# Performance work log

Measured on AMD Instinct MI355X. Metric: run time of the kernel, lower is better.

Reference implementation:

```python
import jax, jax.numpy as jnp
import numpy as np

B, Q, D = 4, 1024, 1024
N, DH = 16, 64  # n_head, d_head
SCALE = 1.0 / DH ** 0.5
LN_EPS = 1e-5


def setup_inputs() -> dict:
    key = jax.random.key(0)
    ks = jax.random.split(key, 10)
    return {
        "w": jax.random.normal(ks[0], (B, Q, D), jnp.float32),
        "r_emb": jax.random.normal(ks[1], (Q, N, DH), jnp.float32),
        "r_w_bias": jax.random.normal(ks[2], (N, DH), jnp.float32),
        "r_bias": jax.random.normal(ks[3], (Q, N), jnp.float32),
        # projection weights stored [in, out]; torch Linear init std = 1/sqrt(d_head)
        "Wq": jax.random.normal(ks[4], (D, N * DH), jnp.float32) * SCALE,
        "Wk": jax.random.normal(ks[5], (D, N * DH), jnp.float32) * SCALE,
        "Wv": jax.random.normal(ks[6], (D, N * DH), jnp.float32) * SCALE,
        "Wo": jax.random.normal(ks[7], (N * DH, D), jnp.float32) * SCALE,
        "ln_gamma": jnp.ones((D,), jnp.float32),
        "ln_beta": jnp.zeros((D,), jnp.float32),
    }


def _rel_shift(x):
    # x: [b, i, j, n]; pad a zero column at the end of j then drop j=0
    # equivalent to shifting left by one along j with a trailing zero.
    return jnp.concatenate([x[:, :, 1:, :], jnp.zeros_like(x[:, :, :1, :])], axis=2)


def reference(w, r_emb, r_w_bias, r_bias, Wq, Wk, Wv, Wo, ln_gamma, ln_beta):
    b, qlen, d = w.shape
    klen = qlen  # mems=None
    n, dh = r_w_bias.shape

    q_h = (w @ Wq).reshape(b, qlen, n, dh)
    k_h = (w @ Wk).reshape(b, klen, n, dh)
    v_h = (w @ Wv).reshape(b, klen, n, dh)

    rw_q = q_h + r_w_bias[None, None]                      # [b,q,n,dh]
    AC = jnp.einsum('bind,bjnd->bijn', rw_q, k_h)          # [b,q,k,n]
    B_ = jnp.einsum('bind,jnd->bijn', q_h, r_emb)          # [b,q,k,n]
    BD = _rel_shift(B_ + r_bias[None, None])               # [b,q,k,n]

    attn_score = (AC + BD) * SCALE
    attn_prob = jax.nn.softmax(attn_score, axis=2)
    attn_vec = jnp.einsum('bijn,bjnd->bind', attn_prob, v_h)
    attn_out = attn_vec.reshape(b, qlen, n * dh) @ Wo

    out = w + attn_out  # residual (post-lnorm path)
    mu = jnp.mean(out, axis=-1, keepdims=True)
    var = jnp.var(out, axis=-1, keepdims=True)
    return (out - mu) / jnp.sqrt(var + LN_EPS) * ln_gamma + ln_beta
```

## Files before the change

kernel.cpp:

```cpp
#include <hip/hip_runtime.h>
#include <hip/hip_bf16.h>

using f16 = _Float16;
typedef _Float16 f16x8 __attribute__((ext_vector_type(8)));
typedef _Float16 f16x4 __attribute__((ext_vector_type(4)));
typedef float f32x4 __attribute__((ext_vector_type(4)));

#define AS1 __attribute__((address_space(1)))
#define AS3 __attribute__((address_space(3)))

constexpr int Bc = 4, Qc = 1024, Dc = 1024, Nh = 16, DHc = 64;
constexpr int BQ = Bc * Qc;
constexpr int NHEAD = Bc * Nh;
constexpr float ATT_SCALE = 0.125f;

__global__ void k_f2h(const float* __restrict__ src, f16* __restrict__ dst) {
    long i8 = ((long)blockIdx.x * blockDim.x + threadIdx.x) * 8;
    float4 a = *(const float4*)&src[i8];
    float4 b = *(const float4*)&src[i8 + 4];
    f16x8 o = { (f16)a.x, (f16)a.y, (f16)a.z, (f16)a.w,
                (f16)b.x, (f16)b.y, (f16)b.z, (f16)b.w };
    *(f16x8*)&dst[i8] = o;
}

struct Ptr4 { const float* p[4]; };
__global__ void k_transpose4(Ptr4 srcs, f16* __restrict__ dst) {
    __shared__ f16 tile[32][33];
    const float* src = srcs.p[blockIdx.z];
    f16* d = dst + (long)blockIdx.z * Dc * Dc;
    int c0 = blockIdx.x * 32, r0 = blockIdx.y * 32;
#pragma unroll
    for (int dy = 0; dy < 32; dy += 8) {
        int r = r0 + threadIdx.y + dy, c = c0 + threadIdx.x;
        tile[threadIdx.y + dy][threadIdx.x] = (f16)src[(long)r * Dc + c];
    }
    __syncthreads();
#pragma unroll
    for (int dy = 0; dy < 32; dy += 8) {
        int c = c0 + threadIdx.y + dy, r = r0 + threadIdx.x;
        d[(long)c * Dc + r] = tile[threadIdx.x][threadIdx.y + dy];
    }
}

__global__ void k_fill_remb(const float* __restrict__ remb, f16* __restrict__ Ke) {
    long gid = (long)blockIdx.x * blockDim.x + threadIdx.x;
    int d8 = (int)(gid & 7) * 8;
    int j = (int)((gid >> 3) & 1023);
    int h = (int)(gid >> 13);
    int n = h & 15;
    f16x8 kv;
    if (j < 1023) {
        const float* rp = &remb[((long)(j + 1) * 16 + n) * 64 + d8];
        float4 r0 = *(const float4*)rp, r1 = *(const float4*)(rp + 4);
        kv[0] = (f16)r0.x; kv[1] = (f16)r0.y; kv[2] = (f16)r0.z; kv[3] = (f16)r0.w;
        kv[4] = (f16)r1.x; kv[5] = (f16)r1.y; kv[6] = (f16)r1.z; kv[7] = (f16)r1.w;
    } else {
        kv = f16x8{};
    }
    *(f16x8*)&Ke[(((long)h << 10) + j) * 64 + d8] = kv;
}

template <int BM, int BN, int BK, int WROWS, int WCOLS, int EPI>
__global__ __launch_bounds__(256) void k_gemm_nt(
    const f16* __restrict__ A, const f16* __restrict__ Bt, void* __restrict__ Cv,
    f16* __restrict__ qtp, f16* __restrict__ ktp, f16* __restrict__ vtp,
    int lda, int ldb, int ldc, int K)
{
    constexpr int TM = BM / (WROWS * 16);
    constexpr int TN = BN / (WCOLS * 16);
    __shared__ __align__(16) f16 sA[BM * BK];
    __shared__ __align__(16) f16 sB[BN * BK];

    const int tid = threadIdx.x;
    const int lane = tid & 63, wave = tid >> 6;
    const int wm = wave / WCOLS, wn = wave % WCOLS;
    const int m0 = blockIdx.y * BM, n0 = blockIdx.x * BN;

    f32x4 acc[TM][TN] = {};

    const int lrow = lane & 15;
    const int kq = (lane >> 4) * 8;
    const int srow = lane >> 2;
    const int scol = (lane & 3) * 8;

    for (int k0 = 0; k0 < K; k0 += BK) {
        __syncthreads();
        constexpr int CHA = BM * BK / 512;
#pragma unroll
        for (int ch = 0; ch < CHA / 4; ++ch) {
            int cc = ch * 4 + wave;
            __builtin_amdgcn_global_load_lds(
                (const AS1 void*)(const void*)&A[(long)(m0 + cc * 16 + srow) * lda + k0 + scol],
                (AS3 void*)(void*)&sA[cc * 512], 16, 0, 0);
        }
        constexpr int CHB = BN * BK / 512;
#pragma unroll
        for (int ch = 0; ch < CHB / 4; ++ch) {
            int cc = ch * 4 + wave;
            __builtin_amdgcn_global_load_lds(
                (const AS1 void*)(const void*)&Bt[(long)(n0 + cc * 16 + srow) * ldb + k0 + scol],
                (AS3 void*)(void*)&sB[cc * 512], 16, 0, 0);
        }
        __syncthreads();

        f16x8 af[TM], bfr[TN];
#pragma unroll
        for (int mi = 0; mi < TM; ++mi)
            af[mi] = *(const f16x8*)&sA[(wm * TM * 16 + mi * 16 + lrow) * BK + kq];
#pragma unroll
        for (int ni = 0; ni < TN; ++ni)
            bfr[ni] = *(const f16x8*)&sB[(wn * TN * 16 + ni * 16 + lrow) * BK + kq];
#pragma unroll
        for (int mi = 0; mi < TM; ++mi)
#pragma unroll
            for (int ni = 0; ni < TN; ++ni)
                acc[mi][ni] = __builtin_amdgcn_mfma_f32_16x16x32_f16(af[mi], bfr[ni], acc[mi][ni], 0, 0, 0);
    }

    const int crow = (lane >> 4) * 4;
    const int ccol = lane & 15;
#pragma unroll
    for (int mi = 0; mi < TM; ++mi)
#pragma unroll
        for (int ni = 0; ni < TN; ++ni)
#pragma unroll
            for (int r = 0; r < 4; ++r) {
                int gm = m0 + wm * TM * 16 + mi * 16 + crow + r;
                int gn = n0 + wn * TN * 16 + ni * 16 + ccol;
                float val = acc[mi][ni][r];
                if constexpr (EPI == 0) {
                    ((f16*)Cv)[(long)gm * ldc + gn] = (f16)val;
                } else {
                    int seg = n0 >> 10;
                    int col = gn & 1023;
                    if (seg == 0) {
                        qtp[(long)gm * 1024 + col] = (f16)val;
                    } else if (seg == 1) {
                        ktp[(long)gm * 1024 + col] = (f16)val;
                    } else {
                        int b = gm >> 10, i = gm & 1023;
                        vtp[(((long)(b << 10) + col) << 10) + i] = (f16)val;
                    }
                }
            }
}

__global__ __launch_bounds__(256, 2) void k_flash(
    const f16* __restrict__ qh, const f16* __restrict__ kh,
    const f16* __restrict__ Ke, const f16* __restrict__ vT,
    const float* __restrict__ rwb, const float* __restrict__ r_bias,
    f16* __restrict__ avp)
{
    constexpr int LDL = 136;
    __shared__ __align__(16) f16 sK[128 * LDL];
    __shared__ __align__(16) f16 sV[64 * LDL];
    __shared__ float sRB[128];

    const int tid = threadIdx.x, lane = tid & 63, wave = tid >> 6;
    const int bid = blockIdx.x;
    const int h = (((bid >> 3) & 7) << 3) | (bid & 7);
    const int i0 = (bid >> 6) * 128;
    const int b = h >> 4, n = h & 15;

    const f16* Vh = vT + (long)h * DHc * Qc;

    const int lrow = lane & 15;
    const int quad = lane >> 4;

    f16x8 rw0, rw1;
#pragma unroll
    for (int e = 0; e < 8; ++e) {
        rw0[e] = (f16)rwb[n * 64 + quad * 8 + e];
        rw1[e] = (f16)rwb[n * 64 + 32 + quad * 8 + e];
    }

    f16x8 aq[2][4];
#pragma unroll
    for (int t = 0; t < 2; ++t) {
        long rix = (long)(b * Qc + i0 + wave * 32 + t * 16 + lrow) * 1024 + n * 64;
        f16x8 q0 = *(const f16x8*)&qh[rix + quad * 8];
        f16x8 q1 = *(const f16x8*)&qh[rix + 32 + quad * 8];
        aq[t][0] = q0 + rw0;
        aq[t][1] = q1 + rw1;
        aq[t][2] = q0;
        aq[t][3] = q1;
    }

    float m_i[2] = {-1e30f, -1e30f}, l_i[2] = {0.0f, 0.0f};
    f32x4 o_acc[2][4] = {};

    for (int j0 = 0; j0 < Qc; j0 += 128) {
        __syncthreads();
        for (int idx = tid; idx < 1024; idx += 256) {
            int r = idx >> 3, c = (idx & 7) * 8;
            *(uint4*)&sK[r * LDL + c] =
                *(const uint4*)&kh[(long)(b * Qc + j0 + r) * 1024 + n * 64 + c];
            *(uint4*)&sK[r * LDL + 64 + c] =
                *(const uint4*)&Ke[((long)h * Qc + j0 + r) * 64 + c];
        }
        for (int idx = tid; idx < 64 * 16; idx += 256) {
            int r = idx >> 4, c = (idx & 15) * 8;
            *(uint4*)&sV[r * LDL + c] = *(const uint4*)&Vh[(long)r * Qc + j0 + c];
        }
        if (tid < 128) {
            int j = j0 + tid;
            sRB[tid] = (j < Qc - 1) ? r_bias[(j + 1) * Nh + n] : 0.0f;
        }
        __syncthreads();

        f32x4 s_acc[2][8] = {};
#pragma unroll
        for (int kc = 0; kc < 4; ++kc)
#pragma unroll
            for (int ni = 0; ni < 8; ++ni) {
                f16x8 bk = *(const f16x8*)&sK[(ni * 16 + lrow) * LDL + kc * 32 + quad * 8];
                s_acc[0][ni] = __builtin_amdgcn_mfma_f32_16x16x32_f16(bk, aq[0][kc], s_acc[0][ni], 0, 0, 0);
                s_acc[1][ni] = __builtin_amdgcn_mfma_f32_16x16x32_f16(bk, aq[1][kc], s_acc[1][ni], 0, 0, 0);
            }

        f16x4 pf[2][8];
        float alpha_t[2];
#pragma unroll
        for (int t = 0; t < 2; ++t) {
            float mx = -1e30f;
#pragma unroll
            for (int ni = 0; ni < 8; ++ni) {
                f32x4 rb4 = *(const f32x4*)&sRB[ni * 16 + quad * 4];
#pragma unroll
                for (int r = 0; r < 4; ++r) {
                    float v = (s_acc[t][ni][r] + rb4[r]) * ATT_SCALE;
                    s_acc[t][ni][r] = v;
                    mx = fmaxf(mx, v);
                }
            }
            mx = fmaxf(mx, __shfl_xor(mx, 16));
            mx = fmaxf(mx, __shfl_xor(mx, 32));
            float mn = fmaxf(m_i[t], mx);
            float alpha = __expf(m_i[t] - mn);
            float sm = 0.0f;
#pragma unroll
            for (int ni = 0; ni < 8; ++ni) {
                float e0 = __expf(s_acc[t][ni][0] - mn);
                float e1 = __expf(s_acc[t][ni][1] - mn);
                float e2 = __expf(s_acc[t][ni][2] - mn);
                float e3 = __expf(s_acc[t][ni][3] - mn);
                sm += (e0 + e1) + (e2 + e3);
                f16x4 pvv; pvv[0] = (f16)e0; pvv[1] = (f16)e1; pvv[2] = (f16)e2; pvv[3] = (f16)e3;
                pf[t][ni] = pvv;
            }
            sm += __shfl_xor(sm, 16);
            sm += __shfl_xor(sm, 32);
            l_i[t] = l_i[t] * alpha + sm;
            m_i[t] = mn;
            alpha_t[t] = alpha;
        }

#pragma unroll
        for (int t = 0; t < 2; ++t)
#pragma unroll
            for (int r = 0; r < 4; ++r) {
                float al = __shfl(alpha_t[t], quad * 4 + r);
#pragma unroll
                for (int dt = 0; dt < 4; ++dt) o_acc[t][dt][r] *= al;
            }

#pragma unroll
        for (int nj = 0; nj < 8; ++nj)
#pragma unroll
            for (int dt = 0; dt < 4; ++dt) {
                f16x4 bv = *(const f16x4*)&sV[(dt * 16 + lrow) * LDL + nj * 16 + quad * 4];
                o_acc[0][dt] = __builtin_amdgcn_mfma_f32_16x16x16f16(pf[0][nj], bv, o_acc[0][dt], 0, 0, 0);
                o_acc[1][dt] = __builtin_amdgcn_mfma_f32_16x16x16f16(pf[1][nj], bv, o_acc[1][dt], 0, 0, 0);
            }
    }

#pragma unroll
    for (int t = 0; t < 2; ++t) {
        float linv = 1.0f / l_i[t];
#pragma unroll
        for (int r = 0; r < 4; ++r) {
            float li = __shfl(linv, quad * 4 + r);
            int i = i0 + wave * 32 + t * 16 + quad * 4 + r;
#pragma unroll
            for (int dt = 0; dt < 4; ++dt) {
                int d = dt * 16 + lrow;
                avp[((long)(b * Qc + i) << 10) + n * 64 + d] = (f16)(o_acc[t][dt][r] * li);
            }
        }
    }
}

__global__ __launch_bounds__(256) void k_res_ln(const float* __restrict__ w, const f16* __restrict__ ao,
                                                const float* __restrict__ gamma, const float* __restrict__ beta,
                                                float* __restrict__ out) {
    const long base = (long)blockIdx.x * 1024;
    const int tid = threadIdx.x;
    float4 wv = *(const float4*)&w[base + tid * 4];
    f16x4 av = *(const f16x4*)&ao[base + tid * 4];
    float x[4] = { wv.x + (float)av[0], wv.y + (float)av[1],
                   wv.z + (float)av[2], wv.w + (float)av[3] };
    float s = x[0] + x[1] + x[2] + x[3];
    float s2 = x[0] * x[0] + x[1] * x[1] + x[2] * x[2] + x[3] * x[3];
#pragma unroll
    for (int off = 32; off; off >>= 1) { s += __shfl_down(s, off); s2 += __shfl_down(s2, off); }
    __shared__ float rs[4], rs2[4];
    if ((tid & 63) == 0) { rs[tid >> 6] = s; rs2[tid >> 6] = s2; }
    __syncthreads();
    s = rs[0] + rs[1] + rs[2] + rs[3];
    s2 = rs2[0] + rs2[1] + rs2[2] + rs2[3];
    float mu = s * (1.0f / 1024.0f);
    float var = s2 * (1.0f / 1024.0f) - mu * mu;
    float inv = rsqrtf(var + 1e-5f);
    float4 gv = *(const float4*)&gamma[tid * 4];
    float4 bv = *(const float4*)&beta[tid * 4];
    float4 o;
    o.x = (x[0] - mu) * inv * gv.x + bv.x;
    o.y = (x[1] - mu) * inv * gv.y + bv.y;
    o.z = (x[2] - mu) * inv * gv.z + bv.z;
    o.w = (x[3] - mu) * inv * gv.w + bv.w;
    *(float4*)&out[base + tid * 4] = o;
}

extern "C" void kernel_launch(void* const* d_in, const int* in_sizes, int n_in,
                              void* d_out, int out_size, void* d_ws, size_t ws_size,
                              hipStream_t stream) {
    const float* w_in   = (const float*)d_in[0];
    const float* r_emb  = (const float*)d_in[1];
    const float* r_wb   = (const float*)d_in[2];
    const float* r_bias = (const float*)d_in[3];
    const float* Wq     = (const float*)d_in[4];
    const float* Wk     = (const float*)d_in[5];
    const float* Wv     = (const float*)d_in[6];
    const float* Wo     = (const float*)d_in[7];
    const float* ln_g   = (const float*)d_in[8];
    const float* ln_b   = (const float*)d_in[9];
    float* out = (float*)d_out;

    char* p = (char*)d_ws;
    auto alloc = [&](size_t bytes) { char* r = p; p += (bytes + 255) & ~(size_t)255; return r; };
    f16* wh = (f16*)alloc((size_t)BQ * Dc * 2);
    f16* WT = (f16*)alloc((size_t)4 * Dc * Dc * 2);
    f16* qh = (f16*)alloc((size_t)BQ * Dc * 2);
    f16* kh = (f16*)alloc((size_t)BQ * Dc * 2);
    f16* Ke = (f16*)alloc((size_t)NHEAD * Qc * DHc * 2);
    f16* vT = (f16*)alloc((size_t)BQ * Dc * 2);
    f16* WoT = WT + (size_t)3 * Dc * Dc;
    f16* avp = wh;
    f16* ao  = Ke;

    k_f2h<<<(BQ * Dc) / (256 * 8), 256, 0, stream>>>(w_in, wh);

    Ptr4 srcs{{Wq, Wk, Wv, Wo}};
    k_transpose4<<<dim3(32, 32, 4), dim3(32, 8), 0, stream>>>(srcs, WT);

    k_fill_remb<<<(NHEAD * Qc * 8) / 256, 256, 0, stream>>>(r_emb, Ke);

    k_gemm_nt<128, 128, 32, 2, 2, 5><<<dim3(3 * Dc / 128, BQ / 128), 256, 0, stream>>>(
        wh, WT, nullptr, qh, kh, vT, Dc, Dc, 0, Dc);

    k_flash<<<512, 256, 0, stream>>>(qh, kh, Ke, vT, r_wb, r_bias, avp);

    k_gemm_nt<64, 128, 32, 2, 2, 0><<<dim3(Dc / 128, BQ / 64), 256, 0, stream>>>(
        avp, WoT, ao, nullptr, nullptr, nullptr, Dc, Dc, Dc, Dc);

    k_res_ln<<<BQ, 256, 0, stream>>>(w_in, ao, ln_g, ln_b, out);
}
```

Baseline: 225.7 us.

## Prefetch next K/V tile into registers during attention compute; fold scale into Q

The attention loop now issues global loads for the next K, Ke, V and r_bias tile into registers before computing on the current tile, then writes them to LDS after the PV MFMAs. This lets global memory latency overlap with compute instead of stalling at the top of each iteration. The softmax scale is also folded into Q, r_w_bias and r_bias, which removes a per-score multiply. The cost is extra registers (12 uint4 per thread), which may reduce occupancy. Scaling Q in fp16 may also change rounding slightly.

Measured after the change: 256.4 us. +13.6%, slower.

```diff
diff --git a/kernel.cpp b/kernel.cpp
--- a/kernel.cpp
+++ b/kernel.cpp
@@ -170,43 +170,76 @@
     f16x8 rw0, rw1;
 #pragma unroll
     for (int e = 0; e < 8; ++e) {
-        rw0[e] = (f16)rwb[n * 64 + quad * 8 + e];
-        rw1[e] = (f16)rwb[n * 64 + 32 + quad * 8 + e];
-    }
-
+        rw0[e] = (f16)(rwb[n * 64 + quad * 8 + e] * ATT_SCALE);
+        rw1[e] = (f16)(rwb[n * 64 + 32 + quad * 8 + e] * ATT_SCALE);
+    }
+
+    const f16 qsc = (f16)0.125f;
     f16x8 aq[2][4];
 #pragma unroll
     for (int t = 0; t < 2; ++t) {
         long rix = (long)(b * Qc + i0 + wave * 32 + t * 16 + lrow) * 1024 + n * 64;
-        f16x8 q0 = *(const f16x8*)&qh[rix + quad * 8];
-        f16x8 q1 = *(const f16x8*)&qh[rix + 32 + quad * 8];
+        f16x8 q0 = *(const f16x8*)&qh[rix + quad * 8] * qsc;
+        f16x8 q1 = *(const f16x8*)&qh[rix + 32 + quad * 8] * qsc;
         aq[t][0] = q0 + rw0;
         aq[t][1] = q1 + rw1;
         aq[t][2] = q0;
         aq[t][3] = q1;
     }
 
+    uint4 rk0[4], rk1[4], rv[4];
+    float rbv;
+
+    auto issue_loads = [&](int j0) {
+#pragma unroll
+        for (int it = 0; it < 4; ++it) {
+            int idx = tid + it * 256;
+            int r = idx >> 3, c = (idx & 7) * 8;
+            rk0[it] = *(const uint4*)&kh[(long)(b * Qc + j0 + r) * 1024 + n * 64 + c];
+            rk1[it] = *(const uint4*)&Ke[((long)h * Qc + j0 + r) * 64 + c];
+        }
+#pragma unroll
+        for (int it = 0; it < 4; ++it) {
+            int idx = tid + it * 256;
+            int r = idx >> 4, c = (idx & 15) * 8;
+            rv[it] = *(const uint4*)&Vh[(long)r * Qc + j0 + c];
+        }
+        rbv = 0.0f;
+        if (tid < 128) {
+            int j = j0 + tid;
+            rbv = (j < Qc - 1) ? r_bias[(j + 1) * Nh + n] * ATT_SCALE : 0.0f;
+        }
+    };
+    auto write_lds = [&]() {
+#pragma unroll
+        for (int it = 0; it < 4; ++it) {
+            int idx = tid + it * 256;
+            int r = idx >> 3, c = (idx & 7) * 8;
+            *(uint4*)&sK[r * LDL + c] = rk0[it];
+            *(uint4*)&sK[r * LDL + 64 + c] = rk1[it];
+        }
+#pragma unroll
+        for (int it = 0; it < 4; ++it) {
+            int idx = tid + it * 256;
+            int r = idx >> 4, c = (idx & 15) * 8;
+            *(uint4*)&sV[r * LDL + c] = rv[it];
+        }
+        if (tid < 128) sRB[tid] = rbv;
+    };
+
     float m_i[2] = {-1e30f, -1e30f}, l_i[2] = {0.0f, 0.0f};
     f32x4 o_acc[2][4] = {};
 
+    issue_loads(0);
+    write_lds();
+    __syncthreads();
+
     for (int j0 = 0; j0 < Qc; j0 += 128) {
-        __syncthreads();
-        for (int idx = tid; idx < 1024; idx += 256) {
-            int r = idx >> 3, c = (idx & 7) * 8;
-            *(uint4*)&sK[r * LDL + c] =
-                *(const uint4*)&kh[(long)(b * Qc + j0 + r) * 1024 + n * 64 + c];
-            *(uint4*)&sK[r * LDL + 64 + c] =
-                *(const uint4*)&Ke[((long)h * Qc + j0 + r) * 64 + c];
-        }
-        for (int idx = tid; idx < 64 * 16; idx += 256) {
-            int r = idx >> 4, c = (idx & 15) * 8;
-            *(uint4*)&sV[r * LDL + c] = *(const uint4*)&Vh[(long)r * Qc + j0 + c];
-        }
-        if (tid < 128) {
-            int j = j0 + tid;
-            sRB[tid] = (j < Qc - 1) ? r_bias[(j + 1) * Nh + n] : 0.0f;
-        }
-        __syncthreads();
+        const bool has_next = (j0 + 128) < Qc;
+        if (has_next) {
+            issue_loads(j0 + 128);
+            __builtin_amdgcn_sched_barrier(0);
+        }
 
         f32x4 s_acc[2][8] = {};
 #pragma unroll
@@ -228,7 +261,7 @@
                 f32x4 rb4 = *(const f32x4*)&sRB[ni * 16 + quad * 4];
 #pragma unroll
                 for (int r = 0; r < 4; ++r) {
-                    float v = (s_acc[t][ni][r] + rb4[r]) * ATT_SCALE;
+                    float v = s_acc[t][ni][r] + rb4[r];
                     s_acc[t][ni][r] = v;
                     mx = fmaxf(mx, v);
                 }
@@ -272,6 +305,12 @@
                 o_acc[0][dt] = __builtin_amdgcn_mfma_f32_16x16x16f16(pf[0][nj], bv, o_acc[0][dt], 0, 0, 0);
                 o_acc[1][dt] = __builtin_amdgcn_mfma_f32_16x16x16f16(pf[1][nj], bv, o_acc[1][dt], 0, 0, 0);
             }
+
+        if (has_next) {
+            __syncthreads();
+            write_lds();
+            __syncthreads();
+        }
     }
 
 #pragma unroll
```

## Split flash attention across 8 waves with 16 query rows each, prefold scale

Applied to the files above, without the earlier changes.

The flash-attention block grows from 4 waves to 8 waves. Each wave now handles 16 query rows instead of 32, which halves the per-wave accumulator and score registers and raises occupancy. The softmax scale is folded into Q, into r_w_bias and into r_bias ahead of time, which removes one multiply per score element. In exchange, each K/V tile is reused by fewer MFMA calls per wave, and the scale is applied in fp16 before the dot product, which changes rounding slightly.

Measured after the change: 218.6 us. 3.1% less time.

```diff
diff --git a/kernel.cpp b/kernel.cpp
--- a/kernel.cpp
+++ b/kernel.cpp
@@ -145,7 +145,7 @@
             }
 }
 
-__global__ __launch_bounds__(256, 2) void k_flash(
+__global__ __launch_bounds__(512, 4) void k_flash(
     const f16* __restrict__ qh, const f16* __restrict__ kh,
     const f16* __restrict__ Ke, const f16* __restrict__ vT,
     const float* __restrict__ rwb, const float* __restrict__ r_bias,
@@ -170,121 +170,111 @@
     f16x8 rw0, rw1;
 #pragma unroll
     for (int e = 0; e < 8; ++e) {
-        rw0[e] = (f16)rwb[n * 64 + quad * 8 + e];
-        rw1[e] = (f16)rwb[n * 64 + 32 + quad * 8 + e];
-    }
-
-    f16x8 aq[2][4];
-#pragma unroll
-    for (int t = 0; t < 2; ++t) {
-        long rix = (long)(b * Qc + i0 + wave * 32 + t * 16 + lrow) * 1024 + n * 64;
-        f16x8 q0 = *(const f16x8*)&qh[rix + quad * 8];
-        f16x8 q1 = *(const f16x8*)&qh[rix + 32 + quad * 8];
-        aq[t][0] = q0 + rw0;
-        aq[t][1] = q1 + rw1;
-        aq[t][2] = q0;
-        aq[t][3] = q1;
-    }
-
-    float m_i[2] = {-1e30f, -1e30f}, l_i[2] = {0.0f, 0.0f};
-    f32x4 o_acc[2][4] = {};
+        rw0[e] = (f16)(rwb[n * 64 + quad * 8 + e] * ATT_SCALE);
+        rw1[e] = (f16)(rwb[n * 64 + 32 + quad * 8 + e] * ATT_SCALE);
+    }
+
+    const f16 qsc = (f16)0.125f;
+    f16x8 aq[4];
+    {
+        long rix = (long)(b * Qc + i0 + wave * 16 + lrow) * 1024 + n * 64;
+        f16x8 q0 = *(const f16x8*)&qh[rix + quad * 8] * qsc;
+        f16x8 q1 = *(const f16x8*)&qh[rix + 32 + quad * 8] * qsc;
+        aq[0] = q0 + rw0;
+        aq[1] = q1 + rw1;
+        aq[2] = q0;
+        aq[3] = q1;
+    }
+
+    float m_i = -1e30f, l_i = 0.0f;
+    f32x4 o_acc[4] = {};
 
     for (int j0 = 0; j0 < Qc; j0 += 128) {
         __syncthreads();
-        for (int idx = tid; idx < 1024; idx += 256) {
+        for (int idx = tid; idx < 1024; idx += 512) {
             int r = idx >> 3, c = (idx & 7) * 8;
             *(uint4*)&sK[r * LDL + c] =
                 *(const uint4*)&kh[(long)(b * Qc + j0 + r) * 1024 + n * 64 + c];
             *(uint4*)&sK[r * LDL + 64 + c] =
                 *(const uint4*)&Ke[((long)h * Qc + j0 + r) * 64 + c];
         }
-        for (int idx = tid; idx < 64 * 16; idx += 256) {
+        for (int idx = tid; idx < 64 * 16; idx += 512) {
             int r = idx >> 4, c = (idx & 15) * 8;
             *(uint4*)&sV[r * LDL + c] = *(const uint4*)&Vh[(long)r * Qc + j0 + c];
         }
         if (tid < 128) {
             int j = j0 + tid;
-            sRB[tid] = (j < Qc - 1) ? r_bias[(j + 1) * Nh + n] : 0.0f;
+            sRB[tid] = (j < Qc - 1) ? r_bias[(j + 1) * Nh + n] * ATT_SCALE : 0.0f;
         }
         __syncthreads();
 
-        f32x4 s_acc[2][8] = {};
+        f32x4 s_acc[8] = {};
 #pragma unroll
         for (int kc = 0; kc < 4; ++kc)
 #pragma unroll
             for (int ni = 0; ni < 8; ++ni) {
                 f16x8 bk = *(const f16x8*)&sK[(ni * 16 + lrow) * LDL + kc * 32 + quad * 8];
-                s_acc[0][ni] = __builtin_amdgcn_mfma_f32_16x16x32_f16(bk, aq[0][kc], s_acc[0][ni], 0, 0, 0);
-                s_acc[1][ni] = __builtin_amdgcn_mfma_f32_16x16x32_f16(bk, aq[1][kc], s_acc[1][ni], 0, 0, 0);
-            }
-
-        f16x4 pf[2][8];
-        float alpha_t[2];
-#pragma unroll
-        for (int t = 0; t < 2; ++t) {
-            float mx = -1e30f;
-#pragma unroll
-            for (int ni = 0; ni < 8; ++ni) {
-                f32x4 rb4 = *(const f32x4*)&sRB[ni * 16 + quad * 4];
-#pragma unroll
-                for (int r = 0; r < 4; ++r) {
-                    float v = (s_acc[t][ni][r] + rb4[r]) * ATT_SCALE;
-                    s_acc[t][ni][r] = v;
-                    mx = fmaxf(mx, v);
-                }
-            }
-            mx = fmaxf(mx, __shfl_xor(mx, 16));
-            mx = fmaxf(mx, __shfl_xor(mx, 32));
-            float mn = fmaxf(m_i[t], mx);
-            float alpha = __expf(m_i[t] - mn);
-            float sm = 0.0f;
-#pragma unroll
-            for (int ni = 0; ni < 8; ++ni) {
-                float e0 = __expf(s_acc[t][ni][0] - mn);
-                float e1 = __expf(s_acc[t][ni][1] - mn);
-                float e2 = __expf(s_acc[t][ni][2] - mn);
-                float e3 = __expf(s_acc[t][ni][3] - mn);
-                sm += (e0 + e1) + (e2 + e3);
-                f16x4 pvv; pvv[0] = (f16)e0; pvv[1] = (f16)e1; pvv[2] = (f16)e2; pvv[3] = (f16)e3;
-                pf[t][ni] = pvv;
-            }
-            sm += __shfl_xor(sm, 16);
-            sm += __shfl_xor(sm, 32);
-            l_i[t] = l_i[t] * alpha + sm;
-            m_i[t] = mn;
-            alpha_t[t] = alpha;
-        }
-
-#pragma unroll
-        for (int t = 0; t < 2; ++t)
+                s_acc[ni] = __builtin_amdgcn_mfma_f32_16x16x32_f16(bk, aq[kc], s_acc[ni], 0, 0, 0);
+            }
+
+        f16x4 pf[8];
+        float mx = -1e30f;
+#pragma unroll
+        for (int ni = 0; ni < 8; ++ni) {
+            f32x4 rb4 = *(const f32x4*)&sRB[ni * 16 + quad * 4];
 #pragma unroll
             for (int r = 0; r < 4; ++r) {
-                float al = __shfl(alpha_t[t], quad * 4 + r);
-#pragma unroll
-                for (int dt = 0; dt < 4; ++dt) o_acc[t][dt][r] *= al;
-            }
+                float v = s_acc[ni][r] + rb4[r];
+                s_acc[ni][r] = v;
+                mx = fmaxf(mx, v);
+            }
+        }
+        mx = fmaxf(mx, __shfl_xor(mx, 16));
+        mx = fmaxf(mx, __shfl_xor(mx, 32));
+        float mn = fmaxf(m_i, mx);
+        float alpha = __expf(m_i - mn);
+        float sm = 0.0f;
+#pragma unroll
+        for (int ni = 0; ni < 8; ++ni) {
+            float e0 = __expf(s_acc[ni][0] - mn);
+            float e1 = __expf(s_acc[ni][1] - mn);
+            float e2 = __expf(s_acc[ni][2] - mn);
+            float e3 = __expf(s_acc[ni][3] - mn);
+            sm += (e0 + e1) + (e2 + e3);
+            f16x4 pvv; pvv[0] = (f16)e0; pvv[1] = (f16)e1; pvv[2] = (f16)e2; pvv[3] = (f16)e3;
+            pf[ni] = pvv;
+        }
+        sm += __shfl_xor(sm, 16);
+        sm += __shfl_xor(sm, 32);
+        l_i = l_i * alpha + sm;
+        m_i = mn;
+
+#pragma unroll
+        for (int r = 0; r < 4; ++r) {
+            float al = __shfl(alpha, quad * 4 + r);
+#pragma unroll
+            for (int dt = 0; dt < 4; ++dt) o_acc[dt][r] *= al;
+        }
 
 #pragma unroll
         for (int nj = 0; nj < 8; ++nj)
 #pragma unroll
             for (int dt = 0; dt < 4; ++dt) {
                 f16x4 bv = *(const f16x4*)&sV[(dt * 16 + lrow) * LDL + nj * 16 + quad * 4];
-                o_acc[0][dt] = __builtin_amdgcn_mfma_f32_16x16x16f16(pf[0][nj], bv, o_acc[0][dt], 0, 0, 0);
-                o_acc[1][dt] = __builtin_amdgcn_mfma_f32_16x16x16f16(pf[1][nj], bv, o_acc[1][dt], 0, 0, 0);
-            }
-    }
-
-#pragma unroll
-    for (int t = 0; t < 2; ++t) {
-        float linv = 1.0f / l_i[t];
+                o_acc[dt] = __builtin_amdgcn_mfma_f32_16x16x16f16(pf[nj], bv, o_acc[dt], 0, 0, 0);
+            }
+    }
+
+    {
+        float linv = 1.0f / l_i;
 #pragma unroll
         for (int r = 0; r < 4; ++r) {
             float li = __shfl(linv, quad * 4 + r);
-            int i = i0 + wave * 32 + t * 16 + quad * 4 + r;
+            int i = i0 + wave * 16 + quad * 4 + r;
 #pragma unroll
             for (int dt = 0; dt < 4; ++dt) {
                 int d = dt * 16 + lrow;
-                avp[((long)(b * Qc + i) << 10) + n * 64 + d] = (f16)(o_acc[t][dt][r] * li);
+                avp[((long)(b * Qc + i) << 10) + n * 64 + d] = (f16)(o_acc[dt][r] * li);
             }
         }
     }
@@ -358,7 +348,7 @@
     k_gemm_nt<128, 128, 32, 2, 2, 5><<<dim3(3 * Dc / 128, BQ / 128), 256, 0, stream>>>(
         wh, WT, nullptr, qh, kh, vT, Dc, Dc, 0, Dc);
 
-    k_flash<<<512, 256, 0, stream>>>(qh, kh, Ke, vT, r_wb, r_bias, avp);
+    k_flash<<<512, 512, 0, stream>>>(qh, kh, Ke, vT, r_wb, r_bias, avp);
 
     k_gemm_nt<64, 128, 32, 2, 2, 0><<<dim3(Dc / 128, BQ / 64), 256, 0, stream>>>(
         avp, WoT, ao, nullptr, nullptr, nullptr, Dc, Dc, Dc, Dc);
```
